# Kernel tuning notes

Hardware: AMD Instinct MI355X
Metric: run time of the kernel (lower is better)

## Reference

```python
import jax, jax.numpy as jnp
import numpy as np

N, E, C, B = 8192, 131072, 256, 64
BINS = 256
CENTERS = jnp.linspace(-6.0, 0.0, BINS)
GAMMA = 255.0 / 6.0  # 1/lengthscale, lengthscale = mean diff of centers = 6/255


def _silu(x):
    return x * jax.nn.sigmoid(x)


def _ln(x, g, b):
    m = x.mean(-1, keepdims=True)
    v = ((x - m) ** 2).mean(-1, keepdims=True)
    return (x - m) / jnp.sqrt(v + 1e-5) * g + b


def _bn(x, g, b):  # training-mode BatchNorm1d (biased var over batch dim)
    m = x.mean(0)
    v = ((x - m) ** 2).mean(0)
    return (x - m) / jnp.sqrt(v + 1e-5) * g + b


def setup_inputs() -> dict:
    key = jax.random.key(0)
    ks = list(jax.random.split(key, 60))
    it = iter(ks)

    def nrm(shape, s=0.05):
        return (jax.random.normal(next(it), shape, dtype=jnp.float32) * s)

    inp = {}
    inp['node'] = jax.random.normal(next(it), (N, 92), dtype=jnp.float32)
    inp['edge_index'] = jax.random.randint(next(it), (2, E), 0, N)
    inp['edge_attr'] = jax.random.normal(next(it), (E, 3), dtype=jnp.float32)
    inp['pdd'] = jax.random.normal(next(it), (N, 51), dtype=jnp.float32)
    inp['batch'] = jnp.sort(jax.random.randint(next(it), (N,), 0, B))
    # atom embedding: Linear(92,C) -> SiLU -> Linear(C,C)
    inp['atom_W1'] = nrm((92, C)); inp['atom_b1'] = jnp.zeros((C,), jnp.float32)
    inp['atom_W2'] = nrm((C, C)); inp['atom_b2'] = jnp.zeros((C,), jnp.float32)
    # edge embedding: RBF(256) -> Linear(256,C) -> SiLU
    inp['edge_W'] = nrm((BINS, C)); inp['edge_b'] = jnp.zeros((C,), jnp.float32)
    # pdd embedding: Linear(51,C)
    inp['pdd_W'] = nrm((51, C)); inp['pdd_b'] = jnp.zeros((C,), jnp.float32)
    # 3 PDDFormerConv layers (Matformer-style), stacked on leading dim
    inp['conv_Wq'] = nrm((3, C, C)); inp['conv_bq'] = jnp.zeros((3, C), jnp.float32)
    inp['conv_Wk'] = nrm((3, C, C)); inp['conv_bk'] = jnp.zeros((3, C), jnp.float32)
    inp['conv_Wv'] = nrm((3, C, C)); inp['conv_bv'] = jnp.zeros((3, C), jnp.float32)
    inp['conv_We'] = nrm((3, C, C)); inp['conv_be'] = jnp.zeros((3, C), jnp.float32)
    inp['conv_Wku'] = nrm((3, 3 * C, C)); inp['conv_bku'] = jnp.zeros((3, C), jnp.float32)
    inp['conv_Wmu'] = nrm((3, 3 * C, C)); inp['conv_bmu'] = jnp.zeros((3, C), jnp.float32)
    inp['conv_Wm'] = nrm((3, C, C)); inp['conv_bm'] = jnp.zeros((3, C), jnp.float32)
    inp['conv_ln_m_g'] = jnp.ones((3, C), jnp.float32); inp['conv_ln_m_b'] = jnp.zeros((3, C), jnp.float32)
    inp['conv_ln_a_g'] = jnp.ones((3, C), jnp.float32); inp['conv_ln_a_b'] = jnp.zeros((3, C), jnp.float32)
    inp['conv_bn_g'] = jnp.ones((3, C), jnp.float32); inp['conv_bn_b'] = jnp.zeros((3, C), jnp.float32)
    # 2 PDD_Conv layers
    inp['pddc_W1'] = nrm((2, C, 2 * C)); inp['pddc_b1'] = jnp.zeros((2, 2 * C), jnp.float32)
    inp['pddc_W2'] = nrm((2, C, C)); inp['pddc_b2'] = jnp.zeros((2, C), jnp.float32)
    inp['pddc_W3'] = nrm((2, C, C)); inp['pddc_b3'] = jnp.zeros((2, C), jnp.float32)
    inp['pddc_bn_g'] = jnp.ones((2, C), jnp.float32); inp['pddc_bn_b'] = jnp.zeros((2, C), jnp.float32)
    # head
    inp['fc_W'] = nrm((C, C)); inp['fc_b'] = jnp.zeros((C,), jnp.float32)
    inp['out_W'] = nrm((C, 1)); inp['out_b'] = jnp.zeros((1,), jnp.float32)
    return inp


def reference(node, edge_index, edge_attr, pdd, batch,
              atom_W1, atom_b1, atom_W2, atom_b2, edge_W, edge_b, pdd_W, pdd_b,
              conv_Wq, conv_bq, conv_Wk, conv_bk, conv_Wv, conv_bv, conv_We, conv_be,
              conv_Wku, conv_bku, conv_Wmu, conv_bmu, conv_Wm, conv_bm,
              conv_ln_m_g, conv_ln_m_b, conv_ln_a_g, conv_ln_a_b, conv_bn_g, conv_bn_b,
              pddc_W1, pddc_b1, pddc_W2, pddc_b2, pddc_W3, pddc_b3, pddc_bn_g, pddc_bn_b,
              fc_W, fc_b, out_W, out_b):
    src, dst = edge_index[0], edge_index[1]
    # embeddings
    x = _silu(node @ atom_W1 + atom_b1) @ atom_W2 + atom_b2            # [N,C]
    d = -1.0 / jnp.linalg.norm(edge_attr, axis=1)                      # [E]
    rbf = jnp.exp(-GAMMA * (d[:, None] - CENTERS) ** 2)                # [E,BINS]
    e_in = _silu(rbf @ edge_W + edge_b)                                # [E,C]
    p = pdd @ pdd_W + pdd_b                                            # [N,C]
    scale = 1.0 / jnp.sqrt(jnp.float32(C))

    def conv(x, i):
        q = x @ conv_Wq[i] + conv_bq[i]
        k = x @ conv_Wk[i] + conv_bk[i]
        v = x @ conv_Wv[i] + conv_bv[i]
        e = e_in @ conv_We[i] + conv_be[i]
        key_e = jnp.concatenate([k[dst], k[src], e], axis=-1) @ conv_Wku[i] + conv_bku[i]
        alpha = q[dst] * key_e * scale
        msg = jnp.concatenate([v[dst], v[src], e], axis=-1) @ conv_Wmu[i] + conv_bmu[i]
        msg = msg * jax.nn.sigmoid(_ln(alpha, conv_ln_a_g[i], conv_ln_a_b[i]))
        msg = _ln(msg @ conv_Wm[i] + conv_bm[i], conv_ln_m_g[i], conv_ln_m_b[i])
        agg = jax.ops.segment_sum(msg, dst, num_segments=N)
        return jax.nn.softplus(x + _bn(agg, conv_bn_g[i], conv_bn_b[i]))

    def pddc(x, adj, i):
        adj = adj + x
        a2 = _bn(adj, pddc_bn_g[i], pddc_bn_b[i]) @ pddc_W1[i] + pddc_b1[i]
        x1, x2 = a2[:, :C], a2[:, C:]
        x1 = x1 @ pddc_W2[i] + pddc_b2[i]
        x2 = jax.nn.gelu(x2, approximate=False)  # dropout inactive at eval
        return (x1 * x2) @ pddc_W3[i] + pddc_b3[i] + x, adj

    x = conv(x, 0)
    x, p = pddc(x, p, 0)
    x = conv(x, 1)
    x, p = pddc(x, p, 1)
    x = conv(x, 2)
    counts = jnp.maximum(jax.ops.segment_sum(jnp.ones((N,), x.dtype), batch, num_segments=B), 1.0)
    pooled = jax.ops.segment_sum(x, batch, num_segments=B) / counts[:, None]
    cf = pooled + _silu(pooled @ fc_W + fc_b)
    return jnp.squeeze(cf @ out_W + out_b)  # [B]
```

## Files before the change

### kernel.cpp

```cpp
#include <hip/hip_runtime.h>
#include <hip/hip_bf16.h>

#define Nn 8192
#define Ne 131072
#define Cc 256
#define Bb 64

typedef __hip_bfloat16 bf16;
typedef __attribute__((ext_vector_type(8))) short bf16x8;
typedef __attribute__((ext_vector_type(4))) float f32x4;

__device__ __forceinline__ float b2f(unsigned short s){
  return __uint_as_float(((unsigned)s) << 16);
}
__device__ __forceinline__ unsigned short f2b(float v){
  bf16 h = __float2bfloat16(v);
  return *(unsigned short*)&h;
}

__device__ __forceinline__ void block_reduce_2(float& s1, float& s2, float* sm){
#pragma unroll
  for (int off = 32; off > 0; off >>= 1){
    s1 += __shfl_down(s1, off, 64);
    s2 += __shfl_down(s2, off, 64);
  }
  int lane = threadIdx.x & 63;
  int wid  = threadIdx.x >> 6;
  if (lane == 0){ sm[wid] = s1; sm[4 + wid] = s2; }
  __syncthreads();
  s1 = sm[0] + sm[1] + sm[2] + sm[3];
  s2 = sm[4] + sm[5] + sm[6] + sm[7];
}

__global__ __launch_bounds__(256) void mg_k(
  const bf16* __restrict__ A,
  const bf16* __restrict__ Bpack, const float* __restrict__ bias,
  bf16* __restrict__ o0, bf16* __restrict__ o1, bf16* __restrict__ o2,
  bf16* __restrict__ o3, bf16* __restrict__ o4,
  float* __restrict__ fout, bf16* __restrict__ foutBf,
  int actMode, const int* __restrict__ outPerm)
{
  int lane = threadIdx.x & 63;
  int wave = threadIdx.x >> 6;
  int panel = blockIdx.x;
  long m0 = (long)blockIdx.y * 64;
  int row16 = lane & 15;
  int kg    = lane >> 4;

  const bf16* a0 = A + (m0 + row16) * 256 + kg * 8;
  const bf16* bp = Bpack + (size_t)panel * 65536;

  f32x4 acc[4][4];
#pragma unroll
  for (int i = 0; i < 4; i++)
#pragma unroll
    for (int j = 0; j < 4; j++) acc[i][j] = (f32x4){0.f, 0.f, 0.f, 0.f};

#pragma unroll
  for (int c8 = 0; c8 < 8; c8++){
    bf16x8 a[4], b[4];
#pragma unroll
    for (int im = 0; im < 4; im++)
      a[im] = *(const bf16x8*)(a0 + im * 4096 + c8 * 32);
#pragma unroll
    for (int in = 0; in < 4; in++)
      b[in] = *(const bf16x8*)(bp + ((size_t)((c8 * 16 + wave * 4 + in) * 64 + lane)) * 8);
#pragma unroll
    for (int im = 0; im < 4; im++)
#pragma unroll
      for (int in = 0; in < 4; in++)
        acc[im][in] = __builtin_amdgcn_mfma_f32_16x16x32_bf16(
                        a[im], b[in], acc[im][in], 0, 0, 0);
  }

  int colq = lane & 15;
  int quad = lane >> 4;

  if (fout){
#pragma unroll
    for (int im = 0; im < 4; im++)
#pragma unroll
      for (int in = 0; in < 4; in++){
        int col = wave * 64 + in * 16 + colq;
        float bv = bias ? bias[col] : 0.f;
#pragma unroll
        for (int r = 0; r < 4; r++){
          long row = m0 + im * 16 + quad * 4 + r;
          float v = acc[im][in][r] + bv + fout[row * 256 + col];
          fout[row * 256 + col] = v;
          if (foutBf) foutBf[row * 256 + col] = __float2bfloat16(v);
        }
      }
    return;
  }

  bf16* op = (panel == 0) ? o0 : (panel == 1) ? o1 : (panel == 2) ? o2
           : (panel == 3) ? o3 : o4;
#pragma unroll
  for (int im = 0; im < 4; im++){
    long orow[4];
#pragma unroll
    for (int r = 0; r < 4; r++){
      long row = m0 + im * 16 + quad * 4 + r;
      orow[r] = outPerm ? (long)outPerm[row] : row;
    }
#pragma unroll
    for (int in = 0; in < 4; in++){
      int col = wave * 64 + in * 16 + colq;
      float bv = bias ? bias[panel * 256 + col] : 0.f;
#pragma unroll
      for (int r = 0; r < 4; r++){
        float v = acc[im][in][r] + bv;
        if (actMode == 1) v = v / (1.f + __expf(-v));
        op[orow[r] * 256 + col] = __float2bfloat16(v);
      }
    }
  }
}

__global__ __launch_bounds__(256) void conv_edge_k(
  const bf16* __restrict__ e_in,
  const bf16* __restrict__ Bedge, const float* __restrict__ bedge,
  const bf16* __restrict__ Bm, const float* __restrict__ bm,
  const bf16* __restrict__ q,
  const bf16* __restrict__ kp1, const bf16* __restrict__ kp2,
  const bf16* __restrict__ vp1, const bf16* __restrict__ vp2,
  const int* __restrict__ dstS, const int* __restrict__ srcS,
  const float* __restrict__ lg, const float* __restrict__ lb,
  bf16* __restrict__ outp)
{
  __shared__ bf16 eK[32 * 256];
  __shared__ bf16 eM[32 * 256];
  int lane = threadIdx.x & 63;
  int wave = threadIdx.x >> 6;
  long m0 = (long)blockIdx.x * 32;
  int row16 = lane & 15;
  int kg    = lane >> 4;
  int colq  = row16;
  int quad  = kg;

  int drs[8], srs[8];
#pragma unroll
  for (int it = 0; it < 8; it++){
    drs[it] = dstS[m0 + it * 4 + wave];
    srs[it] = srcS[m0 + it * 4 + wave];
  }
  int c0g = lane * 4;
  ushort4 k1 = *(const ushort4*)((const unsigned short*)kp1 + (long)drs[0] * 256 + c0g);
  ushort4 k2 = *(const ushort4*)((const unsigned short*)kp2 + (long)srs[0] * 256 + c0g);
  ushort4 qv = *(const ushort4*)((const unsigned short*)q   + (long)drs[0] * 256 + c0g);
  ushort4 v1 = *(const ushort4*)((const unsigned short*)vp1 + (long)drs[0] * 256 + c0g);
  ushort4 v2 = *(const ushort4*)((const unsigned short*)vp2 + (long)srs[0] * 256 + c0g);

  const bf16* a0 = e_in + (m0 + row16) * 256 + kg * 8;

  for (int p = 0; p < 2; p++){
    const bf16* bp = Bedge + (size_t)p * 65536;
    f32x4 acc[2][4];
#pragma unroll
    for (int i = 0; i < 2; i++)
#pragma unroll
      for (int j = 0; j < 4; j++) acc[i][j] = (f32x4){0.f, 0.f, 0.f, 0.f};
#pragma unroll
    for (int c8 = 0; c8 < 8; c8++){
      bf16x8 a[2], b[4];
#pragma unroll
      for (int im = 0; im < 2; im++)
        a[im] = *(const bf16x8*)(a0 + im * 4096 + c8 * 32);
#pragma unroll
      for (int in = 0; in < 4; in++)
        b[in] = *(const bf16x8*)(bp + ((size_t)((c8 * 16 + wave * 4 + in) * 64 + lane)) * 8);
#pragma unroll
      for (int im = 0; im < 2; im++)
#pragma unroll
        for (int in = 0; in < 4; in++)
          acc[im][in] = __builtin_amdgcn_mfma_f32_16x16x32_bf16(
                          a[im], b[in], acc[im][in], 0, 0, 0);
    }
    bf16* E = p ? eM : eK;
    const float* bb = bedge + p * 256;
#pragma unroll
    for (int im = 0; im < 2; im++)
#pragma unroll
      for (int in = 0; in < 4; in++){
        int col = wave * 64 + in * 16 + colq;
        float bv = bb[col];
#pragma unroll
        for (int r = 0; r < 4; r++){
          int row = im * 16 + quad * 4 + r;
          int idx = row * 256 + ((((col >> 3) ^ (row & 7))) << 3) + (col & 7);
          E[idx] = __float2bfloat16(acc[im][in][r] + bv);
        }
      }
  }
  __syncthreads();

  {
    int cb = lane >> 1;
    int e0 = (lane & 1) * 4;
    float4 gv = *(const float4*)(lg + c0g);
    float4 bv = *(const float4*)(lb + c0g);
#pragma unroll
    for (int it = 0; it < 8; it++){
      int row = it * 4 + wave;
      int li = row * 256 + ((cb ^ (row & 7)) << 3) + e0;
      ushort4 ek = *(const ushort4*)((const unsigned short*)eK + li);
      ushort4 em = *(const ushort4*)((const unsigned short*)eM + li);
      ushort4 nk1, nk2, nqv, nv1, nv2;
      if (it < 7){
        long dr2 = drs[it + 1], sr2 = srs[it + 1];
        nk1 = *(const ushort4*)((const unsigned short*)kp1 + dr2 * 256 + c0g);
        nk2 = *(const ushort4*)((const unsigned short*)kp2 + sr2 * 256 + c0g);
        nqv = *(const ushort4*)((const unsigned short*)q   + dr2 * 256 + c0g);
        nv1 = *(const ushort4*)((const unsigned short*)vp1 + dr2 * 256 + c0g);
        nv2 = *(const ushort4*)((const unsigned short*)vp2 + sr2 * 256 + c0g);
      }
      float a0g = (b2f(ek.x) + b2f(k1.x) + b2f(k2.x)) * b2f(qv.x) * 0.0625f;
      float a1g = (b2f(ek.y) + b2f(k1.y) + b2f(k2.y)) * b2f(qv.y) * 0.0625f;
      float a2g = (b2f(ek.z) + b2f(k1.z) + b2f(k2.z)) * b2f(qv.z) * 0.0625f;
      float a3g = (b2f(ek.w) + b2f(k1.w) + b2f(k2.w)) * b2f(qv.w) * 0.0625f;
      float s1 = a0g + a1g + a2g + a3g;
      float s2 = a0g*a0g + a1g*a1g + a2g*a2g + a3g*a3g;
#pragma unroll
      for (int off = 1; off < 64; off <<= 1){
        s1 += __shfl_xor(s1, off, 64);
        s2 += __shfl_xor(s2, off, 64);
      }
      float mn  = s1 * (1.0f / Cc);
      float var = s2 * (1.0f / Cc) - mn * mn;
      float rs  = rsqrtf(var + 1e-5f);
      float g0 = 1.f / (1.f + __expf(-((a0g - mn) * rs * gv.x + bv.x)));
      float g1 = 1.f / (1.f + __expf(-((a1g - mn) * rs * gv.y + bv.y)));
      float g2 = 1.f / (1.f + __expf(-((a2g - mn) * rs * gv.z + bv.z)));
      float g3 = 1.f / (1.f + __expf(-((a3g - mn) * rs * gv.w + bv.w)));
      ushort4 o;
      o.x = f2b((b2f(em.x) + b2f(v1.x) + b2f(v2.x)) * g0);
      o.y = f2b((b2f(em.y) + b2f(v1.y) + b2f(v2.y)) * g1);
      o.z = f2b((b2f(em.z) + b2f(v1.z) + b2f(v2.z)) * g2);
      o.w = f2b((b2f(em.w) + b2f(v1.w) + b2f(v2.w)) * g3);
      *(ushort4*)((unsigned short*)eK + li) = o;
      k1 = nk1; k2 = nk2; qv = nqv; v1 = nv1; v2 = nv2;
    }
  }
  __syncthreads();

  f32x4 acc[2][4];
#pragma unroll
  for (int i = 0; i < 2; i++)
#pragma unroll
    for (int j = 0; j < 4; j++) acc[i][j] = (f32x4){0.f, 0.f, 0.f, 0.f};
  int r7 = row16 & 7;
#pragma unroll
  for (int c8 = 0; c8 < 8; c8++){
    bf16x8 a[2], b[4];
#pragma unroll
    for (int im = 0; im < 2; im++)
      a[im] = *(const bf16x8*)&eK[(row16 + im * 16) * 256 + (((c8 * 4 + kg) ^ r7) << 3)];
#pragma unroll
    for (int in = 0; in < 4; in++)
      b[in] = *(const bf16x8*)(Bm + ((size_t)((c8 * 16 + wave * 4 + in) * 64 + lane)) * 8);
#pragma unroll
    for (int im = 0; im < 2; im++)
#pragma unroll
      for (int in = 0; in < 4; in++)
        acc[im][in] = __builtin_amdgcn_mfma_f32_16x16x32_bf16(
                        a[im], b[in], acc[im][in], 0, 0, 0);
  }

  float s1a[2][4], s2a[2][4];
#pragma unroll
  for (int im = 0; im < 2; im++)
#pragma unroll
    for (int r = 0; r < 4; r++){
      float t1 = 0.f, t2 = 0.f;
#pragma unroll
      for (int in = 0; in < 4; in++){
        int col = wave * 64 + in * 16 + colq;
        float v = acc[im][in][r] + bm[col];
        t1 += v; t2 += v * v;
      }
#pragma unroll
      for (int off = 1; off < 16; off <<= 1){
        t1 += __shfl_xor(t1, off, 64);
        t2 += __shfl_xor(t2, off, 64);
      }
      s1a[im][r] = t1; s2a[im][r] = t2;
    }
  __syncthreads();
  float* red = (float*)eM;
  if (colq < 8){
    int imw = colq >> 2, rw = colq & 3;
    int rr = imw * 16 + quad * 4 + rw;
    red[(wave * 32 + rr) * 2 + 0] = s1a[imw][rw];
    red[(wave * 32 + rr) * 2 + 1] = s2a[imw][rw];
  }
  __syncthreads();
#pragma unroll
  for (int im = 0; im < 2; im++)
#pragma unroll
    for (int r = 0; r < 4; r++){
      int row = im * 16 + quad * 4 + r;
      float ts1 = red[row * 2]           + red[(32 + row) * 2]
                + red[(64 + row) * 2]    + red[(96 + row) * 2];
      float ts2 = red[row * 2 + 1]       + red[(32 + row) * 2 + 1]
                + red[(64 + row) * 2 + 1] + red[(96 + row) * 2 + 1];
      float mn  = ts1 * (1.0f / Cc);
      float var = ts2 * (1.0f / Cc) - mn * mn;
      float rs  = rsqrtf(var + 1e-5f);
      long orow = m0 + row;
#pragma unroll
      for (int in = 0; in < 4; in++){
        int col = wave * 64 + in * 16 + colq;
        float v = acc[im][in][r] + bm[col];
        outp[orow * 256 + col] = __float2bfloat16((v - mn) * rs);
      }
    }
}

__global__ __launch_bounds__(256) void pack_b2_k(
  const float* __restrict__ W, int ldW, bf16* __restrict__ out)
{
  int panel = blockIdx.y;
  long p = (long)blockIdx.x * 256 + threadIdx.x;
  int j    = p & 7;
  int lane = (p >> 3) & 63;
  int nt   = (p >> 9) & 15;
  int kc   = p >> 13;
  int k = kc * 32 + (lane >> 4) * 8 + j;
  int n = nt * 16 + (lane & 15);
  out[(size_t)panel * 65536 + p] =
    __float2bfloat16(W[(long)k * ldW + panel * 256 + n]);
}

__global__ __launch_bounds__(256) void pack_qm_k(
  const float* __restrict__ Wq, const float* __restrict__ Wm,
  bf16* __restrict__ N5, bf16* __restrict__ WpM)
{
  int z = blockIdx.y;
  const float* W; bf16* out;
  if (z < 3){ W = Wq + (size_t)z * 65536; out = N5 + (size_t)z * 327680; }
  else      { W = Wm + (size_t)(z-3) * 65536; out = WpM + (size_t)(z-3) * 65536; }
  long p = (long)blockIdx.x * 256 + threadIdx.x;
  int j    = p & 7;
  int lane = (p >> 3) & 63;
  int nt   = (p >> 9) & 15;
  int kc   = p >> 13;
  int k = kc * 32 + (lane >> 4) * 8 + j;
  int n = nt * 16 + (lane & 15);
  out[p] = __float2bfloat16(W[(long)k * 256 + n]);
}

__global__ __launch_bounds__(256) void fold_k(
  const float* __restrict__ Wk, const float* __restrict__ Wv,
  const float* __restrict__ We,
  const float* __restrict__ Wku, const float* __restrict__ Wmu,
  bf16* __restrict__ N5, bf16* __restrict__ EG)
{
  int z = blockIdx.z, i = z / 6, j = z % 6;
  const float* A; const float* B; bf16* C;
  if (j < 2){
    A = Wk + (size_t)i * 65536; B = Wku + (size_t)i * 196608 + j * 65536;
    C = N5 + (size_t)i * 327680 + (size_t)(1 + j) * 65536;
  } else if (j < 4){
    A = Wv + (size_t)i * 65536; B = Wmu + (size_t)i * 196608 + (j - 2) * 65536;
    C = N5 + (size_t)i * 327680 + (size_t)(3 + (j - 2)) * 65536;
  } else {
    A = We + (size_t)i * 65536;
    B = (j == 4 ? Wku : Wmu) + (size_t)i * 196608 + 131072;
    C = EG + (size_t)i * 131072 + (size_t)(j - 4) * 65536;
  }

  __shared__ __align__(16) float As[16][64];
  __shared__ __align__(16) float Bs[16][128];
  int t = threadIdx.x;
  int m0 = blockIdx.x * 64;
  int n0 = blockIdx.y * 128;

  float acc[4][8];
#pragma unroll
  for (int a = 0; a < 4; a++)
#pragma unroll
    for (int b = 0; b < 8; b++) acc[a][b] = 0.f;
  int tm = t >> 4, tn = t & 15, mA = t & 63, kgA = t >> 6;

  for (int k0 = 0; k0 < 256; k0 += 16){
#pragma unroll
    for (int it = 0; it < 4; it++){
      int kl = kgA + it * 4;
      As[kl][mA] = A[(long)(m0 + mA) * 256 + k0 + kl];
    }
#pragma unroll
    for (int it = 0; it < 8; it++){
      int idx = t + it * 256;
      int kl = idx >> 7, n = idx & 127;
      Bs[kl][n] = B[(long)(k0 + kl) * 256 + n0 + n];
    }
    __syncthreads();
#pragma unroll
    for (int kk = 0; kk < 16; kk++){
      float4 a  = *(const float4*)&As[kk][tm * 4];
      float4 b0 = *(const float4*)&Bs[kk][tn * 4];
      float4 b1 = *(const float4*)&Bs[kk][64 + tn * 4];
      float av[4] = {a.x, a.y, a.z, a.w};
      float bv[8] = {b0.x, b0.y, b0.z, b0.w, b1.x, b1.y, b1.z, b1.w};
#pragma unroll
      for (int ii = 0; ii < 4; ii++)
#pragma unroll
        for (int jj = 0; jj < 8; jj++)
          acc[ii][jj] = __builtin_fmaf(av[ii], bv[jj], acc[ii][jj]);
    }
    __syncthreads();
  }
#pragma unroll
  for (int ii = 0; ii < 4; ii++){
    int m = m0 + tm * 4 + ii;
#pragma unroll
    for (int h = 0; h < 2; h++){
#pragma unroll
      for (int jj = 0; jj < 4; jj++){
        int n = n0 + h * 64 + tn * 4 + jj;
        int kc = m >> 5, nt = n >> 4;
        int ln_ = ((m >> 3) & 3) * 16 + (n & 15);
        long idx = ((long)(kc * 16 + nt) * 64 + ln_) * 8 + (m & 7);
        C[idx] = __float2bfloat16(acc[ii][h * 4 + jj]);
      }
    }
  }
}

__global__ __launch_bounds__(256) void gemm_k(
  const void* __restrict__ A0, int K0, int ld0,
  long M, int Nout,
  const float* __restrict__ W, const float* __restrict__ bias,
  const float* __restrict__ res, int ldRes,
  void* __restrict__ Cout, int outDt, int actMode)
{
  __shared__ __align__(16) float As[16][64];
  __shared__ __align__(16) float Bs[16][128];

  int t = threadIdx.x;
  long m0 = (long)blockIdx.x * 64;
  int  n0 = blockIdx.y * 128;

  float acc[4][8];
#pragma unroll
  for (int i = 0; i < 4; i++)
#pragma unroll
    for (int j = 0; j < 8; j++) acc[i][j] = 0.f;

  int tm = t >> 4, tn = t & 15, mA = t & 63, kgA = t >> 6;
  long rowA = m0 + mA;
  bool rv = rowA < M;

  for (int k0 = 0; k0 < K0; k0 += 16){
#pragma unroll
    for (int it = 0; it < 4; it++){
      int kl = kgA + it * 4;
      int k  = k0 + kl;
      float v = 0.f;
      if (rv && k < K0) v = ((const float*)A0)[rowA * (long)ld0 + k];
      As[kl][mA] = v;
    }
#pragma unroll
    for (int it = 0; it < 8; it++){
      int idx = t + it * 256;
      int kl = idx >> 7, n = idx & 127;
      int k  = k0 + kl;
      Bs[kl][n] = (k < K0) ? W[(long)k * Nout + n0 + n] : 0.f;
    }
    __syncthreads();
#pragma unroll
    for (int kk = 0; kk < 16; kk++){
      float4 a  = *(const float4*)&As[kk][tm * 4];
      float4 b0 = *(const float4*)&Bs[kk][tn * 4];
      float4 b1 = *(const float4*)&Bs[kk][64 + tn * 4];
      float av[4] = {a.x, a.y, a.z, a.w};
      float bv[8] = {b0.x, b0.y, b0.z, b0.w, b1.x, b1.y, b1.z, b1.w};
#pragma unroll
      for (int i = 0; i < 4; i++)
#pragma unroll
        for (int j = 0; j < 8; j++)
          acc[i][j] = __builtin_fmaf(av[i], bv[j], acc[i][j]);
    }
    __syncthreads();
  }

#pragma unroll
  for (int i = 0; i < 4; i++){
    long m = m0 + tm * 4 + i;
    if (m >= M) continue;
#pragma unroll
    for (int h = 0; h < 2; h++){
      int nb = n0 + h * 64 + tn * 4;
      float po[4];
#pragma unroll
      for (int j = 0; j < 4; j++){
        float v = acc[i][h * 4 + j];
        if (bias) v += bias[nb + j];
        if (actMode == 1) v = v / (1.0f + __expf(-v));
        if (res) v += res[m * (long)ldRes + nb + j];
        po[j] = v;
      }
      if (outDt){
        __align__(8) unsigned short tb[4];
#pragma unroll
        for (int j = 0; j < 4; j++) tb[j] = f2b(po[j]);
        *(short4*)((bf16*)Cout + m * (long)Nout + nb) = *(short4*)tb;
      } else {
        float4 ov = {po[0], po[1], po[2], po[3]};
        *(float4*)((float*)Cout + m * (long)Nout + nb) = ov;
      }
    }
  }
}

__global__ __launch_bounds__(256) void zero_k(float* __restrict__ p, long n){
  long i = (long)blockIdx.x * 256 + threadIdx.x;
  long stride = (long)gridDim.x * 256;
  for (; i < n; i += stride) p[i] = 0.f;
}
__global__ __launch_bounds__(256) void zero_i_k(int* __restrict__ p, long n){
  long i = (long)blockIdx.x * 256 + threadIdx.x;
  long stride = (long)gridDim.x * 256;
  for (; i < n; i += stride) p[i] = 0;
}
__global__ __launch_bounds__(256) void f2bf_k(bf16* __restrict__ d,
                                              const float* __restrict__ s, long n){
  long i = (long)blockIdx.x * 256 + threadIdx.x;
  long stride = (long)gridDim.x * 256;
  for (; i < n; i += stride) d[i] = __float2bfloat16(s[i]);
}

__global__ __launch_bounds__(256) void fuse_bias_all_k(
  const float* __restrict__ bku, const float* __restrict__ bmu,
  const float* __restrict__ be,
  const float* __restrict__ bk, const float* __restrict__ bv,
  const float* __restrict__ Wku, const float* __restrict__ Wmu,
  float* __restrict__ b_edge)
{
  int z = blockIdx.x, i = z >> 1, kind = z & 1;
  const float* W  = (kind ? Wmu : Wku) + (size_t)i * 196608;
  const float* b0 = (kind ? bmu : bku) + i * 256;
  const float* vb = (kind ? bv : bk) + i * 256;
  const float* eb = be + i * 256;
  int n = threadIdx.x;
  float s = b0[n];
  for (int k = 0; k < Cc; k++){
    s += eb[k] * W[(512 + k) * 256 + n];
    s += vb[k] * (W[k * 256 + n] + W[(256 + k) * 256 + n]);
  }
  b_edge[i * 512 + kind * 256 + n] = s;
}

__global__ __launch_bounds__(256) void nodeb_all_k(const float* __restrict__ bq,
                                                   float* __restrict__ out){
  int z = blockIdx.x, i = z / 5, p = z % 5;
  out[i * 1280 + p * 256 + threadIdx.x] = (p == 0) ? bq[i * 256 + threadIdx.x] : 0.f;
}

__global__ __launch_bounds__(256) void d_k(const float* __restrict__ ea,
                                           float* __restrict__ d, int E)
{
  int i = blockIdx.x * 256 + threadIdx.x;
  if (i < E){
    float a = ea[i * 3 + 0], b = ea[i * 3 + 1], c = ea[i * 3 + 2];
    d[i] = -rsqrtf(a * a + b * b + c * c);
  }
}

__global__ __launch_bounds__(256) void rbf_k(
  const float* __restrict__ d, bf16* __restrict__ out)
{
  long id = (long)blockIdx.x * 256 + threadIdx.x;
  long m = id >> 8;
  int  k = id & 255;
  float cen = -6.0f + (float)k * (6.0f / 255.0f);
  float df  = d[m] - cen;
  out[id] = __float2bfloat16(__expf(-42.5f * df * df));
}

__global__ __launch_bounds__(256) void hist_k(const int* __restrict__ dst,
                                              int* __restrict__ hist)
{
  int e = blockIdx.x * 256 + threadIdx.x;
  if (e < Ne) atomicAdd(&hist[dst[e]], 1);
}

__global__ __launch_bounds__(1024) void scan_k(
  const int* __restrict__ hist, int* __restrict__ rowptr, int* __restrict__ counter)
{
  __shared__ int part[1024];
  int t = threadIdx.x;
  int base = t * 8;
  int local[8];
  int s = 0;
#pragma unroll
  for (int i = 0; i < 8; i++){ local[i] = s; s += hist[base + i]; }
  part[t] = s;
  __syncthreads();
  for (int off = 1; off < 1024; off <<= 1){
    int v = (t >= off) ? part[t - off] : 0;
    __syncthreads();
    part[t] += v;
    __syncthreads();
  }
  int pre = (t == 0) ? 0 : part[t - 1];
#pragma unroll
  for (int i = 0; i < 8; i++){
    int rp = pre + local[i];
    rowptr[base + i] = rp;
    counter[base + i] = rp;
  }
  if (t == 1023) rowptr[8192] = part[1023];
}

__global__ __launch_bounds__(256) void perm_k(const int* __restrict__ dst,
                                              int* __restrict__ counter,
                                              int* __restrict__ pos)
{
  int e = blockIdx.x * 256 + threadIdx.x;
  if (e < Ne) pos[e] = atomicAdd(&counter[dst[e]], 1);
}

__global__ __launch_bounds__(256) void sortidx_k(
  const int* __restrict__ dst, const int* __restrict__ srcI,
  const int* __restrict__ pos, int* __restrict__ dstS, int* __restrict__ srcS)
{
  int e = blockIdx.x * 256 + threadIdx.x;
  if (e < Ne){
    int p = pos[e];
    dstS[p] = dst[e];
    srcS[p] = srcI[e];
  }
}

__global__ __launch_bounds__(256) void sum_gather_w(
  const bf16* __restrict__ rowsp, const int* __restrict__ rowptr,
  const float* __restrict__ g, const float* __restrict__ b,
  float* __restrict__ agg)
{
  int lane = threadIdx.x & 63;
  long n = (long)blockIdx.x * 4 + (threadIdx.x >> 6);
  int e0 = rowptr[n], e1 = rowptr[n + 1];
  int c0 = lane * 4;
  float t0 = 0.f, t1 = 0.f, t2 = 0.f, t3 = 0.f;
  for (int e = e0; e < e1; e++){
    ushort4 vs = *(const ushort4*)((const unsigned short*)rowsp + (long)e * 256 + c0);
    t0 += b2f(vs.x); t1 += b2f(vs.y); t2 += b2f(vs.z); t3 += b2f(vs.w);
  }
  float cnt = (float)(e1 - e0);
  float4 gv = *(const float4*)(g + c0);
  float4 bv = *(const float4*)(b + c0);
  float4 o = { t0 * gv.x + cnt * bv.x, t1 * gv.y + cnt * bv.y,
               t2 * gv.z + cnt * bv.z, t3 * gv.w + cnt * bv.w };
  *(float4*)(agg + n * 256 + c0) = o;
}

__global__ __launch_bounds__(256) void bn_stats_k(
  const float* __restrict__ X, int rows, float* __restrict__ sums)
{
  int c  = threadIdx.x;
  int r0 = blockIdx.x * 128;
  int re = r0 + 128; if (re > rows) re = rows;
  float s1 = 0.f, s2 = 0.f;
  for (int r = r0; r < re; r++){
    float v = X[(long)r * Cc + c];
    s1 += v; s2 += v * v;
  }
  atomicAdd(&sums[c],      s1);
  atomicAdd(&sums[Cc + c], s2);
}

__global__ __launch_bounds__(256) void bn_apply_softplus_k(
  float* __restrict__ x, bf16* __restrict__ xbf, const float* __restrict__ agg,
  const float* __restrict__ sums,
  const float* __restrict__ g, const float* __restrict__ b)
{
  long r = blockIdx.x;
  int c = threadIdx.x;
  float m    = sums[c] * (1.0f / Nn);
  float var  = sums[Cc + c] * (1.0f / Nn) - m * m;
  float rstd = rsqrtf(var + 1e-5f);
  float bn = (agg[r * Cc + c] - m) * rstd * g[c] + b[c];
  float v  = x[r * Cc + c] + bn;
  float sp = (v > 0.f) ? v + log1pf(__expf(-v)) : log1pf(__expf(v));
  x[r * Cc + c] = sp;
  xbf[r * Cc + c] = __float2bfloat16(sp);
}

__global__ __launch_bounds__(256) void bn_st_k(
  const float* __restrict__ sums, const float* __restrict__ g,
  const float* __restrict__ b, float* __restrict__ S, float* __restrict__ T)
{
  int c = threadIdx.x;
  float m    = sums[c] * (1.0f / Nn);
  float var  = sums[Cc + c] * (1.0f / Nn) - m * m;
  float rstd = rsqrtf(var + 1e-5f);
  S[c] = g[c] * rstd;
  T[c] = b[c] - m * rstd * g[c];
}

__global__ __launch_bounds__(256) void add_k(float* __restrict__ p,
                                             const float* __restrict__ x)
{
  long i = (long)blockIdx.x * 256 + threadIdx.x;
  p[i] += x[i];
}

__global__ __launch_bounds__(256) void bnaff_k(
  const float* __restrict__ p, const float* __restrict__ S,
  const float* __restrict__ T, bf16* __restrict__ out)
{
  long r = blockIdx.x;
  int c = threadIdx.x;
  out[r * 256 + c] = __float2bfloat16(p[r * 256 + c] * S[c] + T[c]);
}

__global__ __launch_bounds__(256) void mulgelu_bf_k(
  bf16* __restrict__ u, const bf16* __restrict__ x1,
  const bf16* __restrict__ a2b)
{
  long r = blockIdx.x;
  int c = threadIdx.x;
  float xg = b2f(*((const unsigned short*)a2b + r * 256 + c));
  float ge = 0.5f * xg * (1.0f + erff(xg * 0.70710678118654752f));
  float x1v = b2f(*((const unsigned short*)x1 + r * 256 + c));
  u[r * 256 + c] = __float2bfloat16(x1v * ge);
}

__global__ __launch_bounds__(256) void pool_k(
  const float* __restrict__ x, const int* __restrict__ batch,
  float* __restrict__ pooled, float* __restrict__ counts)
{
  long r = blockIdx.x;
  int c = threadIdx.x;
  long b = batch[r];
  atomicAdd(&pooled[b * Cc + c], x[r * Cc + c]);
  if (c == 0) atomicAdd(&counts[b], 1.0f);
}

__global__ __launch_bounds__(256) void pooldiv_k(
  float* __restrict__ pooled, const float* __restrict__ counts)
{
  int b = blockIdx.x;
  int c = threadIdx.x;
  float cnt = counts[b];
  if (cnt < 1.f) cnt = 1.f;
  pooled[b * Cc + c] /= cnt;
}

__global__ __launch_bounds__(256) void out_k(
  const float* __restrict__ cf, const float* __restrict__ ow,
  const float* __restrict__ ob, float* __restrict__ out)
{
  __shared__ float sm[8];
  int b = blockIdx.x;
  int c = threadIdx.x;
  float v = cf[(long)b * Cc + c] * ow[c];
  float dummy = 0.f;
  block_reduce_2(v, dummy, sm);
  if (c == 0) out[b] = v + ob[0];
}

static inline void launch_gemm(hipStream_t st,
  const void* A0, int K0, int ld0,
  long M, int Nout, const float* W, const float* bias,
  const float* res, int ldRes, void* Cout, int outDt, int act)
{
  dim3 grid((unsigned)((M + 63) / 64), (unsigned)(Nout / 128));
  gemm_k<<<grid, dim3(256), 0, st>>>(
    A0, K0, ld0, M, Nout, W, bias, res, ldRes, Cout, outDt, act);
}

static inline void launch_mg(hipStream_t st, long M, int panels,
  const bf16* A, const bf16* Bpack, const float* bias,
  bf16* o0, bf16* o1, bf16* o2, bf16* o3, bf16* o4,
  float* fout, bf16* foutBf, int act, const int* outPerm)
{
  dim3 grid((unsigned)panels, (unsigned)(M / 64));
  mg_k<<<grid, dim3(256), 0, st>>>(A, Bpack, bias, o0, o1, o2, o3, o4,
                                   fout, foutBf, act, outPerm);
}

extern "C" void kernel_launch(void* const* d_in, const int* in_sizes, int n_in,
                              void* d_out, int out_size, void* d_ws, size_t ws_size,
                              hipStream_t stream)
{
  (void)in_sizes; (void)n_in; (void)out_size; (void)ws_size;

  const float* node       = (const float*)d_in[0];
  const int*   edge_index = (const int*)  d_in[1];
  const float* edge_attr  = (const float*)d_in[2];
  const float* pdd        = (const float*)d_in[3];
  const int*   batch      = (const int*)  d_in[4];
  const float* atom_W1 = (const float*)d_in[5];
  const float* atom_b1 = (const float*)d_in[6];
  const float* atom_W2 = (const float*)d_in[7];
  const float* atom_b2 = (const float*)d_in[8];
  const float* edge_W  = (const float*)d_in[9];
  const float* edge_b  = (const float*)d_in[10];
  const float* pdd_W   = (const float*)d_in[11];
  const float* pdd_b   = (const float*)d_in[12];
  const float* conv_Wq = (const float*)d_in[13];
  const float* conv_bq = (const float*)d_in[14];
  const float* conv_Wk = (const float*)d_in[15];
  const float* conv_bk = (const float*)d_in[16];
  const float* conv_Wv = (const float*)d_in[17];
  const float* conv_bv = (const float*)d_in[18];
  const float* conv_We = (const float*)d_in[19];
  const float* conv_be = (const float*)d_in[20];
  const float* conv_Wku = (const float*)d_in[21];
  const float* conv_bku = (const float*)d_in[22];
  const float* conv_Wmu = (const float*)d_in[23];
  const float* conv_bmu = (const float*)d_in[24];
  const float* conv_Wm  = (const float*)d_in[25];
  const float* conv_bm  = (const float*)d_in[26];
  const float* ln_m_g = (const float*)d_in[27];
  const float* ln_m_b = (const float*)d_in[28];
  const float* ln_a_g = (const float*)d_in[29];
  const float* ln_a_b = (const float*)d_in[30];
  const float* bn_g   = (const float*)d_in[31];
  const float* bn_b   = (const float*)d_in[32];
  const float* pddc_W1 = (const float*)d_in[33];
  const float* pddc_b1 = (const float*)d_in[34];
  const float* pddc_W2 = (const float*)d_in[35];
  const float* pddc_b2 = (const float*)d_in[36];
  const float* pddc_W3 = (const float*)d_in[37];
  const float* pddc_b3 = (const float*)d_in[38];
  const float* pddc_bn_g = (const float*)d_in[39];
  const float* pddc_bn_b = (const float*)d_in[40];
  const float* fc_W  = (const float*)d_in[41];
  const float* fc_b  = (const float*)d_in[42];
  const float* out_W = (const float*)d_in[43];
  const float* out_b = (const float*)d_in[44];

  const int* src = edge_index;
  const int* dst = edge_index + Ne;

  char* ws = (char*)d_ws;
  size_t off = 0;
  auto alloc = [&](size_t nbytes) -> char* {
    char* ptr = ws + off;
    off += (nbytes + 255) & ~(size_t)255;
    return ptr;
  };
  bf16*  e_in = (bf16*) alloc((size_t)Ne * Cc * 2);
  bf16*  bufB = (bf16*) alloc((size_t)Ne * Cc * 2);
  bf16*  bufC = (bf16*) alloc((size_t)Ne * Cc * 2);
  float* x    = (float*)alloc((size_t)Nn * Cc * 4);
  float* p    = (float*)alloc((size_t)Nn * Cc * 4);
  float* agg  = (float*)alloc((size_t)Nn * Cc * 4);
  bf16*  x_bf  = (bf16*)alloc((size_t)Nn * Cc * 2);
  bf16*  q_bf  = (bf16*)alloc((size_t)Nn * Cc * 2);
  bf16*  kp1   = (bf16*)alloc((size_t)Nn * Cc * 2);
  bf16*  kp2   = (bf16*)alloc((size_t)Nn * Cc * 2);
  bf16*  vp1   = (bf16*)alloc((size_t)Nn * Cc * 2);
  bf16*  vp2   = (bf16*)alloc((size_t)Nn * Cc * 2);
  bf16*  WpN5  = (bf16*)alloc((size_t)3 * 5 * 65536 * 2);
  bf16*  WpEdge= (bf16*)alloc((size_t)3 * 2 * 65536 * 2);
  bf16*  WpM   = (bf16*)alloc((size_t)3 * 65536 * 2);
  bf16*  WpE   = (bf16*)alloc((size_t)65536 * 2);
  bf16*  WpP1  = (bf16*)alloc((size_t)2 * 2 * 65536 * 2);
  bf16*  WpP2  = (bf16*)alloc((size_t)2 * 65536 * 2);
  bf16*  WpP3  = (bf16*)alloc((size_t)2 * 65536 * 2);
  float* nodeb = (float*)alloc((size_t)3 * 1280 * 4);
  float* b_edge= (float*)alloc((size_t)3 * 512 * 4);
  int*   hist    = (int*)alloc((size_t)8192 * 4);
  int*   rowptr  = (int*)alloc((size_t)8193 * 4);
  int*   counter = (int*)alloc((size_t)8192 * 4);
  int*   pos     = (int*)alloc((size_t)Ne * 4);
  int*   dstS    = (int*)alloc((size_t)Ne * 4);
  int*   srcS    = (int*)alloc((size_t)Ne * 4);
  float* pooled = (float*)alloc((size_t)Bb * Cc * 4);
  float* counts = (float*)alloc((size_t)Bb * 4);
  float* cf     = (float*)alloc((size_t)Bb * Cc * 4);
  float* bnsum  = (float*)alloc(2 * Cc * 4);
  float* bnS    = (float*)alloc(Cc * 4);
  float* bnT    = (float*)alloc(Cc * 4);

  float* dArr   = (float*)bufC;
  float* hidden = (float*)(bufC + (size_t)1024 * 1024);
  bf16* a2a = bufC;
  bf16* a2b = bufC + (size_t)Nn * Cc;
  bf16* x1b = bufB;
  bf16* ub  = bufB + (size_t)Nn * Cc;

  zero_i_k<<<dim3(8), dim3(256), 0, stream>>>(hist, 8192);
  hist_k<<<dim3(Ne / 256), dim3(256), 0, stream>>>(dst, hist);
  scan_k<<<dim3(1), dim3(1024), 0, stream>>>(hist, rowptr, counter);
  perm_k<<<dim3(Ne / 256), dim3(256), 0, stream>>>(dst, counter, pos);
  sortidx_k<<<dim3(Ne / 256), dim3(256), 0, stream>>>(dst, src, pos, dstS, srcS);

  d_k<<<dim3((Ne + 255) / 256), dim3(256), 0, stream>>>(edge_attr, dArr, Ne);

  fold_k<<<dim3(4, 2, 18), dim3(256), 0, stream>>>(
    conv_Wk, conv_Wv, conv_We, conv_Wku, conv_Wmu, WpN5, WpEdge);
  pack_qm_k<<<dim3(256, 6), dim3(256), 0, stream>>>(conv_Wq, conv_Wm, WpN5, WpM);
  fuse_bias_all_k<<<dim3(6), dim3(256), 0, stream>>>(
    conv_bku, conv_bmu, conv_be, conv_bk, conv_bv, conv_Wku, conv_Wmu, b_edge);
  nodeb_all_k<<<dim3(15), dim3(256), 0, stream>>>(conv_bq, nodeb);
  pack_b2_k<<<dim3(256, 1), dim3(256), 0, stream>>>(edge_W, 256, WpE);
  for (int j = 0; j < 2; j++){
    pack_b2_k<<<dim3(256, 2), dim3(256), 0, stream>>>(
      pddc_W1 + (size_t)j * 256 * 512, 512, WpP1 + (size_t)j * 2 * 65536);
    pack_b2_k<<<dim3(256, 1), dim3(256), 0, stream>>>(
      pddc_W2 + (size_t)j * 65536, 256, WpP2 + (size_t)j * 65536);
    pack_b2_k<<<dim3(256, 1), dim3(256), 0, stream>>>(
      pddc_W3 + (size_t)j * 65536, 256, WpP3 + (size_t)j * 65536);
  }

  launch_gemm(stream, node, 92, 92, Nn, Cc, atom_W1, atom_b1,
              nullptr, 0, hidden, 0, 1);
  launch_gemm(stream, hidden, 256, 256, Nn, Cc, atom_W2, atom_b2,
              nullptr, 0, x, 0, 0);
  f2bf_k<<<dim3(512), dim3(256), 0, stream>>>(x_bf, x, (long)Nn * Cc);
  launch_gemm(stream, pdd, 51, 51, Nn, Cc, pdd_W, pdd_b,
              nullptr, 0, p, 0, 0);
  rbf_k<<<dim3(Ne), dim3(256), 0, stream>>>(dArr, bufB);
  launch_mg(stream, Ne, 1, bufB, WpE, edge_b,
            e_in, nullptr, nullptr, nullptr, nullptr, nullptr, nullptr, 1, pos);

  for (int i = 0; i < 3; i++){
    launch_mg(stream, Nn, 5, x_bf, WpN5 + (size_t)i * 5 * 65536, nodeb + i * 1280,
              q_bf, kp1, kp2, vp1, vp2, nullptr, nullptr, 0, nullptr);
    conv_edge_k<<<dim3(Ne / 32), dim3(256), 0, stream>>>(
      e_in, WpEdge + (size_t)i * 2 * 65536, b_edge + i * 512,
      WpM + (size_t)i * 65536, conv_bm + i * 256,
      q_bf, kp1, kp2, vp1, vp2, dstS, srcS,
      ln_a_g + i * 256, ln_a_b + i * 256, bufB);
    sum_gather_w<<<dim3(Nn / 4), dim3(256), 0, stream>>>(bufB, rowptr,
              ln_m_g + i * 256, ln_m_b + i * 256, agg);
    zero_k<<<dim3(2), dim3(256), 0, stream>>>(bnsum, 2 * Cc);
    bn_stats_k<<<dim3(Nn / 128), dim3(256), 0, stream>>>(agg, Nn, bnsum);
    bn_apply_softplus_k<<<dim3(Nn), dim3(256), 0, stream>>>(x, x_bf, agg, bnsum,
              bn_g + i * 256, bn_b + i * 256);

    if (i < 2){
      int j = i;
      add_k<<<dim3(Nn * Cc / 256), dim3(256), 0, stream>>>(p, x);
      zero_k<<<dim3(2), dim3(256), 0, stream>>>(bnsum, 2 * Cc);
      bn_stats_k<<<dim3(Nn / 128), dim3(256), 0, stream>>>(p, Nn, bnsum);
      bn_st_k<<<dim3(1), dim3(256), 0, stream>>>(bnsum,
              pddc_bn_g + j * 256, pddc_bn_b + j * 256, bnS, bnT);
      bnaff_k<<<dim3(Nn), dim3(256), 0, stream>>>(p, bnS, bnT, x_bf);
      launch_mg(stream, Nn, 2, x_bf, WpP1 + (size_t)j * 2 * 65536, pddc_b1 + j * 512,
                a2a, a2b, nullptr, nullptr, nullptr, nullptr, nullptr, 0, nullptr);
      launch_mg(stream, Nn, 1, a2a, WpP2 + (size_t)j * 65536, pddc_b2 + j * 256,
                x1b, nullptr, nullptr, nullptr, nullptr, nullptr, nullptr, 0, nullptr);
      mulgelu_bf_k<<<dim3(Nn), dim3(256), 0, stream>>>(ub, x1b, a2b);
      launch_mg(stream, Nn, 1, ub, WpP3 + (size_t)j * 65536, pddc_b3 + j * 256,
                nullptr, nullptr, nullptr, nullptr, nullptr, x, x_bf, 0, nullptr);
    }
  }

  zero_k<<<dim3(64), dim3(256), 0, stream>>>(pooled, (long)Bb * Cc);
  zero_k<<<dim3(1), dim3(256), 0, stream>>>(counts, Bb);
  pool_k<<<dim3(Nn), dim3(256), 0, stream>>>(x, batch, pooled, counts);
  pooldiv_k<<<dim3(Bb), dim3(256), 0, stream>>>(pooled, counts);
  launch_gemm(stream, pooled, 256, 256, Bb, Cc, fc_W, fc_b,
              pooled, Cc, cf, 0, 1);
  out_k<<<dim3(Bb), dim3(256), 0, stream>>>(cf, out_W, out_b, (float*)d_out);
}
```

Measured before the change: 1.682 ms.

## Fuse segment-sum into conv edge kernel via shared-memory run reduction and atomics

The conv edge kernel no longer writes normalized per-edge messages to a global bf16 buffer. It stages them in shared memory, sums runs of equal sorted destinations, and atomically adds the partial sums into an fp32 node aggregate. The LN affine (gamma times sum plus count times beta) moves into the BN stats and apply kernels, and the separate gather kernel goes away. This removes a large per-edge write and read of the message buffer, at the cost of zeroing the aggregate each layer and issuing float atomics, which make the summation order nondeterministic.

```diff
diff --git a/kernel.cpp b/kernel.cpp
--- a/kernel.cpp
+++ b/kernel.cpp
@@ -127,10 +127,11 @@
   const bf16* __restrict__ vp1, const bf16* __restrict__ vp2,
   const int* __restrict__ dstS, const int* __restrict__ srcS,
   const float* __restrict__ lg, const float* __restrict__ lb,
-  bf16* __restrict__ outp)
+  float* __restrict__ aggS)
 {
   __shared__ bf16 eK[32 * 256];
   __shared__ bf16 eM[32 * 256];
+  __shared__ int  sdst[32];
   int lane = threadIdx.x & 63;
   int wave = threadIdx.x >> 6;
   long m0 = (long)blockIdx.x * 32;
@@ -138,6 +139,8 @@
   int kg    = lane >> 4;
   int colq  = row16;
   int quad  = kg;
+
+  if (threadIdx.x < 32) sdst[threadIdx.x] = dstS[m0 + threadIdx.x];
 
   int drs[8], srs[8];
 #pragma unroll
@@ -287,7 +290,7 @@
       s1a[im][r] = t1; s2a[im][r] = t2;
     }
   __syncthreads();
-  float* red = (float*)eM;
+  float* red = (float*)eK;
   if (colq < 8){
     int imw = colq >> 2, rw = colq & 3;
     int rr = imw * 16 + quad * 4 + rw;
@@ -307,14 +310,29 @@
       float mn  = ts1 * (1.0f / Cc);
       float var = ts2 * (1.0f / Cc) - mn * mn;
       float rs  = rsqrtf(var + 1e-5f);
-      long orow = m0 + row;
 #pragma unroll
       for (int in = 0; in < 4; in++){
         int col = wave * 64 + in * 16 + colq;
         float v = acc[im][in][r] + bm[col];
-        outp[orow * 256 + col] = __float2bfloat16((v - mn) * rs);
-      }
-    }
+        ((unsigned short*)eM)[row * 256 + col] = f2b((v - mn) * rs);
+      }
+    }
+  __syncthreads();
+
+  {
+    int t = threadIdx.x;
+    float sum = 0.f;
+    int cur = sdst[0];
+    for (int r = 0; r < 32; r++){
+      int d = sdst[r];
+      if (d != cur){
+        atomicAdd(&aggS[(long)cur * 256 + t], sum);
+        sum = 0.f; cur = d;
+      }
+      sum += b2f(((const unsigned short*)eM)[r * 256 + t]);
+    }
+    atomicAdd(&aggS[(long)cur * 256 + t], sum);
+  }
 }
 
 __global__ __launch_bounds__(256) void pack_b2_k(
@@ -634,26 +652,43 @@
   }
 }
 
-__global__ __launch_bounds__(256) void sum_gather_w(
-  const bf16* __restrict__ rowsp, const int* __restrict__ rowptr,
-  const float* __restrict__ g, const float* __restrict__ b,
-  float* __restrict__ agg)
-{
-  int lane = threadIdx.x & 63;
-  long n = (long)blockIdx.x * 4 + (threadIdx.x >> 6);
-  int e0 = rowptr[n], e1 = rowptr[n + 1];
-  int c0 = lane * 4;
-  float t0 = 0.f, t1 = 0.f, t2 = 0.f, t3 = 0.f;
-  for (int e = e0; e < e1; e++){
-    ushort4 vs = *(const ushort4*)((const unsigned short*)rowsp + (long)e * 256 + c0);
-    t0 += b2f(vs.x); t1 += b2f(vs.y); t2 += b2f(vs.z); t3 += b2f(vs.w);
-  }
-  float cnt = (float)(e1 - e0);
-  float4 gv = *(const float4*)(g + c0);
-  float4 bv = *(const float4*)(b + c0);
-  float4 o = { t0 * gv.x + cnt * bv.x, t1 * gv.y + cnt * bv.y,
-               t2 * gv.z + cnt * bv.z, t3 * gv.w + cnt * bv.w };
-  *(float4*)(agg + n * 256 + c0) = o;
+__global__ __launch_bounds__(256) void bn_stats_f(
+  const float* __restrict__ S, const int* __restrict__ rowptr,
+  const float* __restrict__ lg, const float* __restrict__ lb,
+  float* __restrict__ sums)
+{
+  int c  = threadIdx.x;
+  int r0 = blockIdx.x * 128;
+  float gc = lg[c], bc = lb[c];
+  float s1 = 0.f, s2 = 0.f;
+  for (int r = r0; r < r0 + 128; r++){
+    float cnt = (float)(rowptr[r + 1] - rowptr[r]);
+    float y = gc * S[(long)r * Cc + c] + cnt * bc;
+    s1 += y; s2 += y * y;
+  }
+  atomicAdd(&sums[c],      s1);
+  atomicAdd(&sums[Cc + c], s2);
+}
+
+__global__ __launch_bounds__(256) void bn_apply_softplus_f(
+  float* __restrict__ x, bf16* __restrict__ xbf,
+  const float* __restrict__ S, const int* __restrict__ rowptr,
+  const float* __restrict__ lg, const float* __restrict__ lb,
+  const float* __restrict__ sums,
+  const float* __restrict__ g, const float* __restrict__ b)
+{
+  long r = blockIdx.x;
+  int c = threadIdx.x;
+  float cnt = (float)(rowptr[r + 1] - rowptr[r]);
+  float y = lg[c] * S[r * Cc + c] + cnt * lb[c];
+  float m    = sums[c] * (1.0f / Nn);
+  float var  = sums[Cc + c] * (1.0f / Nn) - m * m;
+  float rstd = rsqrtf(var + 1e-5f);
+  float bn = (y - m) * rstd * g[c] + b[c];
+  float v  = x[r * Cc + c] + bn;
+  float sp = (v > 0.f) ? v + log1pf(__expf(-v)) : log1pf(__expf(v));
+  x[r * Cc + c] = sp;
+  xbf[r * Cc + c] = __float2bfloat16(sp);
 }
 
 __global__ __launch_bounds__(256) void bn_stats_k(
@@ -669,23 +704,6 @@
   }
   atomicAdd(&sums[c],      s1);
   atomicAdd(&sums[Cc + c], s2);
-}
-
-__global__ __launch_bounds__(256) void bn_apply_softplus_k(
-  float* __restrict__ x, bf16* __restrict__ xbf, const float* __restrict__ agg,
-  const float* __restrict__ sums,
-  const float* __restrict__ g, const float* __restrict__ b)
-{
-  long r = blockIdx.x;
-  int c = threadIdx.x;
-  float m    = sums[c] * (1.0f / Nn);
-  float var  = sums[Cc + c] * (1.0f / Nn) - m * m;
-  float rstd = rsqrtf(var + 1e-5f);
-  float bn = (agg[r * Cc + c] - m) * rstd * g[c] + b[c];
-  float v  = x[r * Cc + c] + bn;
-  float sp = (v > 0.f) ? v + log1pf(__expf(-v)) : log1pf(__expf(v));
-  x[r * Cc + c] = sp;
-  xbf[r * Cc + c] = __float2bfloat16(sp);
 }
 
 __global__ __launch_bounds__(256) void bn_st_k(
@@ -923,16 +941,17 @@
   for (int i = 0; i < 3; i++){
     launch_mg(stream, Nn, 5, x_bf, WpN5 + (size_t)i * 5 * 65536, nodeb + i * 1280,
               q_bf, kp1, kp2, vp1, vp2, nullptr, nullptr, 0, nullptr);
+    zero_k<<<dim3(1024), dim3(256), 0, stream>>>(agg, (long)Nn * Cc);
     conv_edge_k<<<dim3(Ne / 32), dim3(256), 0, stream>>>(
       e_in, WpEdge + (size_t)i * 2 * 65536, b_edge + i * 512,
       WpM + (size_t)i * 65536, conv_bm + i * 256,
       q_bf, kp1, kp2, vp1, vp2, dstS, srcS,
-      ln_a_g + i * 256, ln_a_b + i * 256, bufB);
-    sum_gather_w<<<dim3(Nn / 4), dim3(256), 0, stream>>>(bufB, rowptr,
-              ln_m_g + i * 256, ln_m_b + i * 256, agg);
+      ln_a_g + i * 256, ln_a_b + i * 256, agg);
     zero_k<<<dim3(2), dim3(256), 0, stream>>>(bnsum, 2 * Cc);
-    bn_stats_k<<<dim3(Nn / 128), dim3(256), 0, stream>>>(agg, Nn, bnsum);
-    bn_apply_softplus_k<<<dim3(Nn), dim3(256), 0, stream>>>(x, x_bf, agg, bnsum,
+    bn_stats_f<<<dim3(Nn / 128), dim3(256), 0, stream>>>(agg, rowptr,
+              ln_m_g + i * 256, ln_m_b + i * 256, bnsum);
+    bn_apply_softplus_f<<<dim3(Nn), dim3(256), 0, stream>>>(x, x_bf, agg, rowptr,
+              ln_m_g + i * 256, ln_m_b + i * 256, bnsum,
               bn_g + i * 256, bn_b + i * 256);
 
     if (i < 2){
```

Measured after the change: 1.614 ms. 4.0% less time.
